# Kernel optimization log

Hardware: AMD Instinct MI355X
Metric: run time of the kernel (lower is better)

Reference implementation:

```python
import jax, jax.numpy as jnp
import numpy as np

# Semantics of GPTQ Marlin 2:4 int4 GEMM: W_dense[K,N] has exactly 2 nonzeros per
# group of 4 along K. Compressed int4 values (q-8)*scale are stored packed 8-per-int32
# in B [K/16, N]; meta [K/4, N] in [0,6) selects which pair of the 4 positions is
# nonzero (index into the 6 combinations). s [K/groupsize, N] are group scales.

_PAIRS = jnp.array([[0, 1], [0, 2], [0, 3], [1, 2], [1, 3], [2, 3]], dtype=jnp.int32)


def _dequant_24(B, meta, s):
    Kd16, N = B.shape
    K = Kd16 * 16
    # unpack 8 nibbles per int32 -> [K/2, N] compressed values
    shifts = (jnp.arange(8, dtype=jnp.int32) * 4)[None, :, None]
    nib = (B[:, None, :] >> shifts) & 0xF            # [K/16, 8, N]
    vals = nib.reshape(K // 2, N).astype(jnp.float32) - 8.0  # symmetric zero-point 8
    gs = K // s.shape[0]                              # original groupsize
    scale = jnp.repeat(s, gs // 2, axis=0)            # [K/2, N] (compressed K dim)
    deq = (vals * scale).reshape(K // 4, 2, N)        # 2 values per group of 4
    pos = _PAIRS[meta]                                # [K/4, N, 2] positions in [0,4)
    oh = jax.nn.one_hot(pos, 4, dtype=jnp.float32)    # [K/4, N, 2, 4]
    W = jnp.einsum('gjn,gnjp->gpn', deq, oh)          # scatter into group slots
    return W.reshape(K, N)


def setup_inputs() -> dict:
    key = jax.random.key(0)
    k0, k1, k2, k3, k4 = jax.random.split(key, 5)
    M, K, N, GS = 8192, 4096, 4096, 128
    A = jax.random.normal(k0, (M, K), dtype=jnp.float32)
    B = jax.random.randint(k1, (K // 16, N), 0, 2147483647, dtype=jnp.int32)
    meta = jax.random.randint(k2, (K // 4, N), 0, 6, dtype=jnp.int32)
    s = jax.random.uniform(k3, (K // GS, N), dtype=jnp.float32, minval=0.005, maxval=0.02)
    bias = jax.random.normal(k4, (N,), dtype=jnp.float32)
    return {"A": A, "B": B, "meta": meta, "s": s, "bias": bias}


def reference(A, B, meta, s, bias):
    W = _dequant_24(B, meta, s)          # [K, N] dense 2:4-sparse dequantized weight
    return jnp.matmul(A, W, preferred_element_type=jnp.float32) + bias
```

## Files before the change

### kernel.cpp

```cpp
#include <hip/hip_runtime.h>

typedef _Float16 h16;
typedef __attribute__((ext_vector_type(8))) _Float16 h16x8;
typedef __attribute__((ext_vector_type(4))) float f32x4;
typedef unsigned int u32;

#define BARRIER() __builtin_amdgcn_s_barrier()
#define SCHEDB()  __builtin_amdgcn_sched_barrier(0)
#define VMCNT_(n) asm volatile("s_waitcnt vmcnt(" #n ")" ::: "memory")
#define VMCNT(n)  VMCNT_(n)

__global__ __launch_bounds__(256) void cvtA_kernel(const float* __restrict__ A,
                                                   h16* __restrict__ Ah, int total8) {
  int stride = gridDim.x * blockDim.x;
  for (int i = blockIdx.x * blockDim.x + threadIdx.x; i < total8; i += stride) {
    const f32x4* p = (const f32x4*)(A + (size_t)i * 8);
    f32x4 v0 = p[0], v1 = p[1];
    h16x8 o;
    o[0] = (h16)v0[0]; o[1] = (h16)v0[1]; o[2] = (h16)v0[2]; o[3] = (h16)v0[3];
    o[4] = (h16)v1[0]; o[5] = (h16)v1[1]; o[6] = (h16)v1[2]; o[7] = (h16)v1[3];
    *(h16x8*)(Ah + (size_t)i * 8) = o;
  }
}

__global__ __launch_bounds__(256) void dequant_kernel(const int* __restrict__ Bq,
    const int* __restrict__ meta, const float* __restrict__ s,
    h16* __restrict__ Wt, int K, int N, int chunksPerGroup) {
  int n = blockIdx.x * 256 + threadIdx.x;
  int chunk = blockIdx.y;
  u32 w0 = (u32)Bq[(size_t)(chunk * 2) * N + n];
  u32 w1 = (u32)Bq[(size_t)(chunk * 2 + 1) * N + n];
  float sc = s[(size_t)(chunk / chunksPerGroup) * N + n];
  h16 out[32];
#pragma unroll
  for (int gi = 0; gi < 8; ++gi) {
    int g = chunk * 8 + gi;
    int mm = meta[(size_t)g * N + n];
    u32 w = (gi < 4) ? w0 : w1;
    int j0 = (2 * gi) & 7;
    float d0 = (float)((int)((w >> (4 * j0)) & 0xFu) - 8) * sc;
    float d1 = (float)((int)((w >> (4 * j0 + 4)) & 0xFu) - 8) * sc;
    u32 enc = (0xED9C84u >> (4 * mm)) & 0xFu;
    int p0 = (int)(enc & 3u), p1 = (int)(enc >> 2);
#pragma unroll
    for (int p = 0; p < 4; ++p) {
      float v = (p == p0) ? d0 : ((p == p1) ? d1 : 0.0f);
      out[gi * 4 + p] = (h16)v;
    }
  }
  h16* dst = Wt + (size_t)n * K + chunk * 32;
  *(h16x8*)(dst + 0)  = *(h16x8*)(out + 0);
  *(h16x8*)(dst + 8)  = *(h16x8*)(out + 8);
  *(h16x8*)(dst + 16) = *(h16x8*)(out + 16);
  *(h16x8*)(dst + 24) = *(h16x8*)(out + 24);
}

__device__ __forceinline__ void rd4(h16x8 (&d)[4][2], const h16* base, int row,
                                    int s0, int s1) {
#pragma unroll
  for (int m = 0; m < 4; ++m) {
    d[m][0] = *(const h16x8*)(base + row + m * 1024 + s0);
    d[m][1] = *(const h16x8*)(base + row + m * 1024 + s1);
  }
}
__device__ __forceinline__ void rd2(h16x8 (&d)[2][2], const h16* base, int row,
                                    int s0, int s1) {
#pragma unroll
  for (int n = 0; n < 2; ++n) {
    d[n][0] = *(const h16x8*)(base + row + n * 1024 + s0);
    d[n][1] = *(const h16x8*)(base + row + n * 1024 + s1);
  }
}
__device__ __forceinline__ void mmaQ(f32x4 (&acc)[8][4], int mo, int no,
                                     const h16x8 (&a)[4][2], const h16x8 (&b)[2][2]) {
#pragma unroll
  for (int m = 0; m < 4; ++m)
#pragma unroll
    for (int n = 0; n < 2; ++n) {
      acc[mo + m][no + n] = __builtin_amdgcn_mfma_f32_16x16x32_f16(a[m][0], b[n][0], acc[mo + m][no + n], 0, 0, 0);
      acc[mo + m][no + n] = __builtin_amdgcn_mfma_f32_16x16x32_f16(a[m][1], b[n][1], acc[mo + m][no + n], 0, 0, 0);
    }
}

__global__ __launch_bounds__(512, 2) void gemm_kernel(const h16* __restrict__ A,
    const h16* __restrict__ Wt, const float* __restrict__ bias,
    float* __restrict__ C, int M, int N, int K) {
  __shared__ alignas(16) h16 As[2 * 2 * 8192];
  __shared__ alignas(16) h16 Bs[2 * 2 * 8192];

  const int nTilesN = N >> 8;
  const int nwg = gridDim.x;
  int bid = blockIdx.x;
  int wg = (bid & 7) * (nwg >> 3) + (bid >> 3);
  int tm = wg / nTilesN, tn = wg - tm * nTilesN;

  const int tid = threadIdx.x;
  const int lane = tid & 63, w = tid >> 6;
  const int wr = w >> 2, wc = w & 3;

  const int i0 = tid >> 3;
  const int sigma = (tid & 7) ^ ((tid >> 3) & 7);
  const h16* gA_t = A + ((size_t)(tm * 256) + i0) * K + sigma * 8;
  const int rB0 = ((i0 >> 5) << 6) + (i0 & 31);
  const h16* gB_t = Wt + ((size_t)(tn * 256) + rB0) * K + sigma * 8;
  const int tid8 = tid * 8;
  const size_t rowK128 = (size_t)128 * K;

#define GLOAD(SRC, DST) __builtin_amdgcn_global_load_lds(                      \
    (const __attribute__((address_space(1))) void*)(SRC),                      \
    (__attribute__((address_space(3))) void*)(DST), 16, 0, 0)

#define STAGE_A(T_, mh_) do {                                                  \
    const h16* s_ = gA_t + (size_t)((mh_) * 64) * K + (T_) * 64;               \
    h16* d_ = As + ((((T_) & 1) * 2 + (mh_)) * 8192) + tid8;                   \
    GLOAD(s_, d_); GLOAD(s_ + rowK128, d_ + 4096); } while (0)

#define STAGE_B(T_, nh_) do {                                                  \
    const h16* s_ = gB_t + (size_t)((nh_) * 32) * K + (T_) * 64;               \
    h16* d_ = Bs + ((((T_) & 1) * 2 + (nh_)) * 8192) + tid8;                   \
    GLOAD(s_, d_); GLOAD(s_ + rowK128, d_ + 4096); } while (0)

  const int ln15 = lane & 15, l16 = lane >> 4, l7 = lane & 7;
  const int aRow = (wr * 64 + ln15) * 64;
  const int bRow = (wc * 32 + ln15) * 64;
  const int sl0 = ((0 + l16) ^ l7) * 8;
  const int sl1 = ((4 + l16) ^ l7) * 8;

  f32x4 acc[8][4] = {};
  h16x8 afA[4][2], bX[2][2], bY[2][2];
  const int NT = K >> 6;
  const int NTh = NT >> 1;

  STAGE_A(0, 0); STAGE_B(0, 0); STAGE_B(0, 1); STAGE_A(0, 1);
  STAGE_A(1, 0); STAGE_B(1, 0); STAGE_B(1, 1);
  VMCNT(10);
  BARRIER();
  rd2(bX, Bs, bRow, sl0, sl1);
  SCHEDB();
  VMCNT(8);
  BARRIER();

#define TILE(T_, A0_, A1_, B1_, B0n_, H0_, H1_, G1_, G_, GR_, V1_, V2_, V3_, V4_) do { \
                                                             \
    rd4(afA, A0_, aRow, sl0, sl1);                                \
    rd2(H1_, B1_, bRow, sl0, sl1);                                \
    if (G1_) STAGE_A((T_) + 1, 1);                                             \
    SCHEDB(); VMCNT(V1_); BARRIER();                                           \
    __builtin_amdgcn_s_setprio(1); mmaQ(acc, 0, 0, afA, H0_);                  \
    __builtin_amdgcn_s_setprio(0); SCHEDB(); BARRIER();                        \
                                                             \
    if (G_) STAGE_A((T_) + 2, 0);                                              \
    SCHEDB(); VMCNT(V2_); BARRIER();                                           \
    __builtin_amdgcn_s_setprio(1); mmaQ(acc, 0, 2, afA, H1_);                  \
    __builtin_amdgcn_s_setprio(0); SCHEDB(); BARRIER();                        \
                                                             \
    rd4(afA, A1_, aRow, sl0, sl1);                                \
    if (G_) STAGE_B((T_) + 2, 0);                                              \
    SCHEDB(); VMCNT(V3_); BARRIER();                                           \
    __builtin_amdgcn_s_setprio(1); mmaQ(acc, 4, 2, afA, H1_);                  \
    __builtin_amdgcn_s_setprio(0); SCHEDB(); BARRIER();                        \
                                                             \
    if (GR_) rd2(H1_, B0n_, bRow, sl0, sl1);          \
    if (G_) STAGE_B((T_) + 2, 1);                                              \
    SCHEDB(); VMCNT(V4_); BARRIER();                                           \
    __builtin_amdgcn_s_setprio(1); mmaQ(acc, 4, 0, afA, H0_);                  \
    __builtin_amdgcn_s_setprio(0); SCHEDB(); BARRIER();                        \
  } while (0)

  for (int it = 0; it < NTh - 1; ++it) {
    const int T = it * 2;
    TILE(T,     As,         As + 8192,  Bs + 8192,  Bs + 16384, bX, bY,
         true, true, true, 8, 8, 8, 8);
    TILE(T + 1, As + 16384, As + 24576, Bs + 24576, Bs,         bY, bX,
         true, true, true, 8, 8, 8, 8);
  }
  {
    const int T = NT - 2;
    TILE(T,     As,         As + 8192,  Bs + 8192,  Bs + 16384, bX, bY,
         true,  false, true,  8, 8, 4, 2);
    TILE(T + 1, As + 16384, As + 24576, Bs + 24576, Bs,         bY, bX,
         false, false, false, 0, 0, 0, 0);
  }

  int colBase = tn * 256 + wc * 64 + ln15;
  int rowBase = tm * 256 + wr * 128 + l16 * 4;
#pragma unroll
  for (int n = 0; n < 4; ++n) {
    float bv = bias[colBase + n * 16];
#pragma unroll
    for (int m = 0; m < 8; ++m) {
#pragma unroll
      for (int j = 0; j < 4; ++j) {
        C[(size_t)(rowBase + m * 16 + j) * N + colBase + n * 16] = acc[m][n][j] + bv;
      }
    }
  }
#undef TILE
#undef STAGE_A
#undef STAGE_B
#undef GLOAD
}

extern "C" void kernel_launch(void* const* d_in, const int* in_sizes, int n_in,
                              void* d_out, int out_size, void* d_ws, size_t ws_size,
                              hipStream_t stream) {
  const float* A = (const float*)d_in[0];
  const int* Bq = (const int*)d_in[1];
  const int* meta = (const int*)d_in[2];
  const float* s = (const float*)d_in[3];
  const float* bias = (const float*)d_in[4];
  float* C = (float*)d_out;

  const int N = in_sizes[4];
  const int K = (int)(((long long)in_sizes[1] * 16) / N);
  const int M = (int)((long long)in_sizes[0] / K);
  const int sRows = (int)((long long)in_sizes[3] / N);
  const int chunksPerGroup = (K / sRows) / 32;

  h16* Ah = (h16*)d_ws;
  h16* Wt = Ah + (size_t)M * K;

  cvtA_kernel<<<2048, 256, 0, stream>>>(A, Ah, (M * K) / 8);

  dim3 dgrid(N / 256, K / 32);
  dequant_kernel<<<dgrid, 256, 0, stream>>>(Bq, meta, s, Wt, K, N, chunksPerGroup);

  int grid = (M / 256) * (N / 256);
  gemm_kernel<<<grid, 512, 0, stream>>>(Ah, Wt, bias, C, M, N, K);
}
```

Baseline: 324.5 us.

## Load B fragments directly from global into registers, deepen A LDS ring

B fragments are now read straight from global memory into registers, one k-tile ahead, instead of being staged through LDS. All of LDS goes to a four-deep ring of A tiles. The per-tile schedule shrinks from four barrier phases to two, and tile traversal becomes N-major (tn outer, tm inner). This removes B's LDS traffic and some barriers, but adds uncoalesced direct global loads for B, higher register pressure, and vmcnt accounting that mixes B loads with A staging.

```diff
diff --git a/kernel.cpp b/kernel.cpp
--- a/kernel.cpp
+++ b/kernel.cpp
@@ -55,7 +55,7 @@
   *(h16x8*)(dst + 24) = *(h16x8*)(out + 24);
 }
 
-__device__ __forceinline__ void rd4(h16x8 (&d)[4][2], const h16* base, int row,
+__device__ __forceinline__ void rdA(h16x8 (&d)[4][2], const h16* base, int row,
                                     int s0, int s1) {
 #pragma unroll
   for (int m = 0; m < 4; ++m) {
@@ -63,36 +63,35 @@
     d[m][1] = *(const h16x8*)(base + row + m * 1024 + s1);
   }
 }
-__device__ __forceinline__ void rd2(h16x8 (&d)[2][2], const h16* base, int row,
-                                    int s0, int s1) {
-#pragma unroll
-  for (int n = 0; n < 2; ++n) {
-    d[n][0] = *(const h16x8*)(base + row + n * 1024 + s0);
-    d[n][1] = *(const h16x8*)(base + row + n * 1024 + s1);
-  }
-}
-__device__ __forceinline__ void mmaQ(f32x4 (&acc)[8][4], int mo, int no,
-                                     const h16x8 (&a)[4][2], const h16x8 (&b)[2][2]) {
+__device__ __forceinline__ void loadB(h16x8 (&b)[4][2], const h16* Wb, size_t K, int T) {
+#pragma unroll
+  for (int n = 0; n < 4; ++n)
+#pragma unroll
+    for (int ks = 0; ks < 2; ++ks)
+      b[n][ks] = *(const h16x8*)(Wb + (size_t)n * 16 * K + ks * 32 + (size_t)T * 64);
+}
+__device__ __forceinline__ void mfma32(f32x4 (&acc)[8][4], int mo,
+                                       const h16x8 (&a)[4][2], const h16x8 (&b)[4][2]) {
 #pragma unroll
   for (int m = 0; m < 4; ++m)
 #pragma unroll
-    for (int n = 0; n < 2; ++n) {
-      acc[mo + m][no + n] = __builtin_amdgcn_mfma_f32_16x16x32_f16(a[m][0], b[n][0], acc[mo + m][no + n], 0, 0, 0);
-      acc[mo + m][no + n] = __builtin_amdgcn_mfma_f32_16x16x32_f16(a[m][1], b[n][1], acc[mo + m][no + n], 0, 0, 0);
+    for (int n = 0; n < 4; ++n) {
+      acc[mo + m][n] = __builtin_amdgcn_mfma_f32_16x16x32_f16(a[m][0], b[n][0], acc[mo + m][n], 0, 0, 0);
+      acc[mo + m][n] = __builtin_amdgcn_mfma_f32_16x16x32_f16(a[m][1], b[n][1], acc[mo + m][n], 0, 0, 0);
     }
 }
 
 __global__ __launch_bounds__(512, 2) void gemm_kernel(const h16* __restrict__ A,
     const h16* __restrict__ Wt, const float* __restrict__ bias,
     float* __restrict__ C, int M, int N, int K) {
-  __shared__ alignas(16) h16 As[2 * 2 * 8192];
-  __shared__ alignas(16) h16 Bs[2 * 2 * 8192];
-
-  const int nTilesN = N >> 8;
+  __shared__ alignas(16) h16 As[4 * 2 * 8192];
+
+  const size_t Kl = (size_t)K;
+  const int nTilesM = M >> 8;
   const int nwg = gridDim.x;
   int bid = blockIdx.x;
   int wg = (bid & 7) * (nwg >> 3) + (bid >> 3);
-  int tm = wg / nTilesN, tn = wg - tm * nTilesN;
+  int tn = wg / nTilesM, tm = wg - tn * nTilesM;
 
   const int tid = threadIdx.x;
   const int lane = tid & 63, w = tid >> 6;
@@ -100,87 +99,61 @@
 
   const int i0 = tid >> 3;
   const int sigma = (tid & 7) ^ ((tid >> 3) & 7);
-  const h16* gA_t = A + ((size_t)(tm * 256) + i0) * K + sigma * 8;
-  const int rB0 = ((i0 >> 5) << 6) + (i0 & 31);
-  const h16* gB_t = Wt + ((size_t)(tn * 256) + rB0) * K + sigma * 8;
+  const h16* gA_t = A + ((size_t)(tm * 256) + i0) * Kl + sigma * 8;
   const int tid8 = tid * 8;
-  const size_t rowK128 = (size_t)128 * K;
+  const size_t rowK128 = (size_t)128 * Kl;
+  h16* AsF = As;
 
 #define GLOAD(SRC, DST) __builtin_amdgcn_global_load_lds(                      \
     (const __attribute__((address_space(1))) void*)(SRC),                      \
     (__attribute__((address_space(3))) void*)(DST), 16, 0, 0)
 
-#define STAGE_A(T_, mh_) do {                                                  \
-    const h16* s_ = gA_t + (size_t)((mh_) * 64) * K + (T_) * 64;               \
-    h16* d_ = As + ((((T_) & 1) * 2 + (mh_)) * 8192) + tid8;                   \
-    GLOAD(s_, d_); GLOAD(s_ + rowK128, d_ + 4096); } while (0)
-
-#define STAGE_B(T_, nh_) do {                                                  \
-    const h16* s_ = gB_t + (size_t)((nh_) * 32) * K + (T_) * 64;               \
-    h16* d_ = Bs + ((((T_) & 1) * 2 + (nh_)) * 8192) + tid8;                   \
+#define STAGE_A(T_, h_) do {                                                   \
+    const h16* s_ = gA_t + (size_t)((h_) * 64) * Kl + (size_t)(T_) * 64;       \
+    h16* d_ = AsF + ((((T_) & 3) * 2 + (h_)) * 8192) + tid8;                   \
     GLOAD(s_, d_); GLOAD(s_ + rowK128, d_ + 4096); } while (0)
 
   const int ln15 = lane & 15, l16 = lane >> 4, l7 = lane & 7;
   const int aRow = (wr * 64 + ln15) * 64;
-  const int bRow = (wc * 32 + ln15) * 64;
   const int sl0 = ((0 + l16) ^ l7) * 8;
   const int sl1 = ((4 + l16) ^ l7) * 8;
 
+  const h16* Wb = Wt + ((size_t)(tn * 256 + wc * 64 + ln15)) * Kl + l16 * 8;
+
   f32x4 acc[8][4] = {};
-  h16x8 afA[4][2], bX[2][2], bY[2][2];
+  h16x8 af[4][2], bX[4][2], bY[4][2];
   const int NT = K >> 6;
-  const int NTh = NT >> 1;
-
-  STAGE_A(0, 0); STAGE_B(0, 0); STAGE_B(0, 1); STAGE_A(0, 1);
-  STAGE_A(1, 0); STAGE_B(1, 0); STAGE_B(1, 1);
-  VMCNT(10);
-  BARRIER();
-  rd2(bX, Bs, bRow, sl0, sl1);
-  SCHEDB();
-  VMCNT(8);
-  BARRIER();
-
-#define TILE(T_, A0_, A1_, B1_, B0n_, H0_, H1_, G1_, G_, GR_, V1_, V2_, V3_, V4_) do { \
+
+  loadB(bX, Wb, Kl, 0);
+  STAGE_A(0, 0); STAGE_A(0, 1); STAGE_A(1, 0); STAGE_A(1, 1);
+  SCHEDB(); VMCNT(4); BARRIER(); SCHEDB();
+
+#define TILE(T_, BCUR, BNXT, GB_, GS_, VM_P2) do {                             \
+    const h16* aH0 = AsF + (((T_) & 3) * 2 + 0) * 8192;                        \
+    const h16* aH1 = AsF + (((T_) & 3) * 2 + 1) * 8192;                        \
                                                              \
-    rd4(afA, A0_, aRow, sl0, sl1);                                \
-    rd2(H1_, B1_, bRow, sl0, sl1);                                \
-    if (G1_) STAGE_A((T_) + 1, 1);                                             \
-    SCHEDB(); VMCNT(V1_); BARRIER();                                           \
-    __builtin_amdgcn_s_setprio(1); mmaQ(acc, 0, 0, afA, H0_);                  \
-    __builtin_amdgcn_s_setprio(0); SCHEDB(); BARRIER();                        \
+    rdA(af, aH0, aRow, sl0, sl1);                                              \
+    if (GB_) loadB(BNXT, Wb, Kl, (T_) + 1);                                    \
+    if (GS_) STAGE_A((T_) + 2, 0);                                             \
+    SCHEDB();                                                                  \
+    __builtin_amdgcn_s_setprio(1); mfma32(acc, 0, af, BCUR);                   \
+    __builtin_amdgcn_s_setprio(0);                                             \
+    SCHEDB(); BARRIER(); SCHEDB();                                             \
                                                              \
-    if (G_) STAGE_A((T_) + 2, 0);                                              \
-    SCHEDB(); VMCNT(V2_); BARRIER();                                           \
-    __builtin_amdgcn_s_setprio(1); mmaQ(acc, 0, 2, afA, H1_);                  \
-    __builtin_amdgcn_s_setprio(0); SCHEDB(); BARRIER();                        \
-                                                             \
-    rd4(afA, A1_, aRow, sl0, sl1);                                \
-    if (G_) STAGE_B((T_) + 2, 0);                                              \
-    SCHEDB(); VMCNT(V3_); BARRIER();                                           \
-    __builtin_amdgcn_s_setprio(1); mmaQ(acc, 4, 2, afA, H1_);                  \
-    __builtin_amdgcn_s_setprio(0); SCHEDB(); BARRIER();                        \
-                                                             \
-    if (GR_) rd2(H1_, B0n_, bRow, sl0, sl1);          \
-    if (G_) STAGE_B((T_) + 2, 1);                                              \
-    SCHEDB(); VMCNT(V4_); BARRIER();                                           \
-    __builtin_amdgcn_s_setprio(1); mmaQ(acc, 4, 0, afA, H0_);                  \
-    __builtin_amdgcn_s_setprio(0); SCHEDB(); BARRIER();                        \
+    rdA(af, aH1, aRow, sl0, sl1);                                              \
+    if (GS_) STAGE_A((T_) + 2, 1);                                             \
+    SCHEDB(); VM_P2; BARRIER(); SCHEDB();                                      \
+    __builtin_amdgcn_s_setprio(1); mfma32(acc, 4, af, BCUR);                   \
+    __builtin_amdgcn_s_setprio(0); SCHEDB();                                   \
   } while (0)
 
-  for (int it = 0; it < NTh - 1; ++it) {
+  for (int it = 0; it < (NT - 2) / 2; ++it) {
     const int T = it * 2;
-    TILE(T,     As,         As + 8192,  Bs + 8192,  Bs + 16384, bX, bY,
-         true, true, true, 8, 8, 8, 8);
-    TILE(T + 1, As + 16384, As + 24576, Bs + 24576, Bs,         bY, bX,
-         true, true, true, 8, 8, 8, 8);
-  }
-  {
-    const int T = NT - 2;
-    TILE(T,     As,         As + 8192,  Bs + 8192,  Bs + 16384, bX, bY,
-         true,  false, true,  8, 8, 4, 2);
-    TILE(T + 1, As + 16384, As + 24576, Bs + 24576, Bs,         bY, bX,
-         false, false, false, 0, 0, 0, 0);
-  }
+    TILE(T,     bX, bY, true, true, VMCNT(14));
+    TILE(T + 1, bY, bX, true, true, VMCNT(14));
+  }
+  TILE(NT - 2, bX, bY, true,  false, VMCNT(10));
+  TILE(NT - 1, bY, bX, false, false, (void)0);
 
   int colBase = tn * 256 + wc * 64 + ln15;
   int rowBase = tm * 256 + wr * 128 + l16 * 4;
@@ -197,7 +170,6 @@
   }
 #undef TILE
 #undef STAGE_A
-#undef STAGE_B
 #undef GLOAD
 }
 
```

New measurement: 468.7 us. 44.5% more time.

## Double-buffer A fragments in registers and move vmcnt waits after MMAs

Applied to the files above, without the earlier changes.

Splits the A fragment registers into two sets (aH0/aH1) and adds a third B fragment set, so LDS reads for the next quarter-tile are issued a phase earlier and overlap the current MFMA block. The global-load wait counters now sit after each MMA phase instead of before it, so waits on in-flight loads can be hidden behind compute. The cost is extra VGPR pressure from the additional fragment buffers, which could lower occupancy or cause spills. The loop tail is also restructured with explicit per-phase wait counts.

```diff
diff --git a/kernel.cpp b/kernel.cpp
--- a/kernel.cpp
+++ b/kernel.cpp
@@ -127,60 +127,54 @@
   const int sl1 = ((4 + l16) ^ l7) * 8;
 
   f32x4 acc[8][4] = {};
-  h16x8 afA[4][2], bX[2][2], bY[2][2];
+  h16x8 aH0[4][2], aH1[4][2], bX[2][2], bY[2][2], bZ[2][2];
   const int NT = K >> 6;
-  const int NTh = NT >> 1;
 
   STAGE_A(0, 0); STAGE_B(0, 0); STAGE_B(0, 1); STAGE_A(0, 1);
   STAGE_A(1, 0); STAGE_B(1, 0); STAGE_B(1, 1);
-  VMCNT(10);
-  BARRIER();
+  VMCNT(10); SCHEDB(); BARRIER();
+  rd4(aH0, As, aRow, sl0, sl1);
   rd2(bX, Bs, bRow, sl0, sl1);
-  SCHEDB();
-  VMCNT(8);
-  BARRIER();
-
-#define TILE(T_, A0_, A1_, B1_, B0n_, H0_, H1_, G1_, G_, GR_, V1_, V2_, V3_, V4_) do { \
-                                                             \
-    rd4(afA, A0_, aRow, sl0, sl1);                                \
-    rd2(H1_, B1_, bRow, sl0, sl1);                                \
+  SCHEDB(); VMCNT(8); SCHEDB(); BARRIER();
+
+#define TILE(T_, A1c, A0n, B1c, B0n, BF0, BSP, G1_, G2_, VM1, VM2, VM3, VM4) do { \
+                                                                       \
+    rd2(bY, B1c, bRow, sl0, sl1);                                              \
     if (G1_) STAGE_A((T_) + 1, 1);                                             \
-    SCHEDB(); VMCNT(V1_); BARRIER();                                           \
-    __builtin_amdgcn_s_setprio(1); mmaQ(acc, 0, 0, afA, H0_);                  \
-    __builtin_amdgcn_s_setprio(0); SCHEDB(); BARRIER();                        \
-                                                             \
-    if (G_) STAGE_A((T_) + 2, 0);                                              \
-    SCHEDB(); VMCNT(V2_); BARRIER();                                           \
-    __builtin_amdgcn_s_setprio(1); mmaQ(acc, 0, 2, afA, H1_);                  \
-    __builtin_amdgcn_s_setprio(0); SCHEDB(); BARRIER();                        \
-                                                             \
-    rd4(afA, A1_, aRow, sl0, sl1);                                \
-    if (G_) STAGE_B((T_) + 2, 0);                                              \
-    SCHEDB(); VMCNT(V3_); BARRIER();                                           \
-    __builtin_amdgcn_s_setprio(1); mmaQ(acc, 4, 2, afA, H1_);                  \
-    __builtin_amdgcn_s_setprio(0); SCHEDB(); BARRIER();                        \
-                                                             \
-    if (GR_) rd2(H1_, B0n_, bRow, sl0, sl1);          \
-    if (G_) STAGE_B((T_) + 2, 1);                                              \
-    SCHEDB(); VMCNT(V4_); BARRIER();                                           \
-    __builtin_amdgcn_s_setprio(1); mmaQ(acc, 4, 0, afA, H0_);                  \
-    __builtin_amdgcn_s_setprio(0); SCHEDB(); BARRIER();                        \
+    SCHEDB(); BARRIER();                                                       \
+    __builtin_amdgcn_s_setprio(1); mmaQ(acc, 0, 0, aH0, BF0);                  \
+    __builtin_amdgcn_s_setprio(0); VM1; SCHEDB(); BARRIER();                   \
+                                                                       \
+    rd4(aH1, A1c, aRow, sl0, sl1);                                             \
+    if (G2_) STAGE_A((T_) + 2, 0);                                             \
+    SCHEDB(); BARRIER();                                                       \
+    __builtin_amdgcn_s_setprio(1); mmaQ(acc, 0, 2, aH0, bY);                   \
+    __builtin_amdgcn_s_setprio(0); VM2; SCHEDB(); BARRIER();                   \
+                                                                       \
+    if (G1_) rd4(aH0, A0n, aRow, sl0, sl1);                                    \
+    if (G2_) STAGE_B((T_) + 2, 0);                                             \
+    SCHEDB(); BARRIER();                                                       \
+    __builtin_amdgcn_s_setprio(1); mmaQ(acc, 4, 2, aH1, bY);                   \
+    __builtin_amdgcn_s_setprio(0); VM3; SCHEDB(); BARRIER();                   \
+                                                                       \
+    if (G1_) rd2(BSP, B0n, bRow, sl0, sl1);                                    \
+    if (G2_) STAGE_B((T_) + 2, 1);                                             \
+    SCHEDB(); BARRIER();                                                       \
+    __builtin_amdgcn_s_setprio(1); mmaQ(acc, 4, 0, aH1, BF0);                  \
+    __builtin_amdgcn_s_setprio(0); VM4; SCHEDB(); BARRIER();                   \
   } while (0)
 
-  for (int it = 0; it < NTh - 1; ++it) {
+  for (int it = 0; it < (NT - 2) / 2; ++it) {
     const int T = it * 2;
-    TILE(T,     As,         As + 8192,  Bs + 8192,  Bs + 16384, bX, bY,
-         true, true, true, 8, 8, 8, 8);
-    TILE(T + 1, As + 16384, As + 24576, Bs + 24576, Bs,         bY, bX,
-         true, true, true, 8, 8, 8, 8);
-  }
-  {
-    const int T = NT - 2;
-    TILE(T,     As,         As + 8192,  Bs + 8192,  Bs + 16384, bX, bY,
-         true,  false, true,  8, 8, 4, 2);
-    TILE(T + 1, As + 16384, As + 24576, Bs + 24576, Bs,         bY, bX,
-         false, false, false, 0, 0, 0, 0);
-  }
+    TILE(T,     As + 8192,  As + 16384, Bs + 8192,  Bs + 16384, bX, bZ,
+         true, true, VMCNT(8), VMCNT(8), VMCNT(8), VMCNT(8));
+    TILE(T + 1, As + 24576, As,         Bs + 24576, Bs,         bZ, bX,
+         true, true, VMCNT(8), VMCNT(8), VMCNT(8), VMCNT(8));
+  }
+  TILE(NT - 2, As + 8192,  As + 16384, Bs + 8192,  Bs + 16384, bX, bZ,
+       true,  false, VMCNT(8), VMCNT(6), VMCNT(4), VMCNT(2));
+  TILE(NT - 1, As + 24576, As,         Bs + 24576, Bs,         bZ, bX,
+       false, false, VMCNT(0), (void)0, (void)0, (void)0);
 
   int colBase = tn * 256 + wc * 64 + ln15;
   int rowBase = tm * 256 + wr * 128 + l16 * 4;
```

After: 908.0 us. +179.9%, slower.
